# Optimization experiments

Hardware: AMD Instinct MI355X
Metric: run time of the kernel (lower is better)

## Reference

```python
import jax, jax.numpy as jnp
import numpy as np

B, S, D = 8, 2048, 256


def setup_inputs() -> dict:
    key = jax.random.key(0)
    ks = jax.random.split(key, 8)
    sc = 0.05
    return {
        "q": jax.random.normal(ks[0], (B, S, D), jnp.float32),
        "k": jax.random.normal(ks[1], (B, S, D), jnp.float32),
        "v": jax.random.normal(ks[2], (B, S, D), jnp.float32),
        "Wi0": jax.random.normal(ks[3], (D, D), jnp.float32) * sc,
        "Wi1": jax.random.normal(ks[4], (D, D), jnp.float32) * sc,
        "Wo0": jax.random.normal(ks[5], (D, D), jnp.float32) * sc,
        "Wo1": jax.random.normal(ks[6], (D, D), jnp.float32) * sc,
        "bo0": jnp.zeros((D,), jnp.float32),
        "bo1": jnp.zeros((D,), jnp.float32),
    }


def reference(q, k, v, Wi0, Wi1, Wo0, Wo1, bo0, bo1):
    d = q.shape[-1]
    scale = 1.0 / np.sqrt(d).astype(np.float32)
    # (B, S, S) shared score matrix
    scores = jnp.einsum("bqd,bkd->bqk", q, k) * scale
    s = scores.shape[-1]
    i = jnp.arange(s)[:, None]
    j = jnp.arange(s)[None, :]
    NEG = jnp.float32(-1e9)
    # fw: mask strictly-lower triangle (attend to j >= i); bw: mask strictly-upper (j <= i)
    fw_w = jax.nn.softmax(jnp.where(j < i, NEG, scores), axis=-1)
    bw_w = jax.nn.softmax(jnp.where(j > i, NEG, scores), axis=-1)
    fw_v = jnp.einsum("bqk,bkd->bqd", fw_w, v)
    bw_v = jnp.einsum("bqk,bkd->bqd", bw_w, v)
    # fusion gates: sigmoid(in_gate(v) + out_gate(att_v))  (torch Linear: x @ W.T + b)
    fw_gate = jax.nn.sigmoid(v @ Wi0.T + fw_v @ Wo0.T + bo0)
    bw_gate = jax.nn.sigmoid(v @ Wi1.T + bw_v @ Wo1.T + bo1)
    fw_out = fw_gate * fw_v + (1.0 - fw_gate) * v
    bw_out = bw_gate * bw_v + (1.0 - bw_gate) * v
    return jnp.concatenate((fw_out, bw_out), axis=-1)
```

## Files before the change

kernel.cpp:

```cpp
#include <hip/hip_runtime.h>
#include <stdint.h>


typedef unsigned short u16;
typedef unsigned int u32;
typedef __attribute__((ext_vector_type(8))) short short8;
typedef __attribute__((ext_vector_type(4))) float f32x4;

#define B_ 8
#define S_ 2048
#define D_ 256
#define QB 64
#define NP 32

#define LOG2E 1.44269504088896340736f
#define QSCALE (LOG2E/16.0f)
#define KSWZ_OFF 0
#define VT_OFF   (8u<<20)
#define WBF_OFF  (16u<<20)

__device__ __forceinline__ u16 f2bf(float f) {
    union { float f; u32 u; } x; x.f = f;
    u32 u = x.u + 0x7fffu + ((x.u >> 16) & 1u);
    return (u16)(u >> 16);
}
__device__ __forceinline__ float fget(float4 v, int i) {
    return i == 0 ? v.x : i == 1 ? v.y : i == 2 ? v.z : v.w;
}
__device__ __forceinline__ short8 pack8(float4 a, float4 b) {
    short8 r;
    r[0] = (short)f2bf(a.x); r[1] = (short)f2bf(a.y);
    r[2] = (short)f2bf(a.z); r[3] = (short)f2bf(a.w);
    r[4] = (short)f2bf(b.x); r[5] = (short)f2bf(b.y);
    r[6] = (short)f2bf(b.z); r[7] = (short)f2bf(b.w);
    return r;
}
__device__ __forceinline__ f32x4 mfma16(short8 a, short8 b, f32x4 c) {
    return __builtin_amdgcn_mfma_f32_16x16x32_bf16(a, b, c, 0, 0, 0);
}
__device__ __forceinline__ void gload_lds(const void* g, void* lds) {
    __builtin_amdgcn_global_load_lds(
        (const __attribute__((address_space(1))) void*)g,
        (__attribute__((address_space(3))) void*)lds, 16, 0, 0);
}

__global__ __launch_bounds__(256, 1)
void prep_kernel(const float* __restrict__ k, const float* __restrict__ v,
                 const float* __restrict__ w0, const float* __restrict__ w1,
                 const float* __restrict__ w2, const float* __restrict__ w3,
                 char* __restrict__ ws)
{
    const int tid = (int)threadIdx.x;
    const int bid = (int)blockIdx.x;

    if (bid < 512) {
        __shared__ float vs[32][257];
        const int b = bid >> 6, jt = bid & 63;
        const float* vb = v + ((size_t)b * S_ + (size_t)jt * 32) * D_;
        const int j = tid >> 3, d0 = (tid & 7) * 32;
        #pragma unroll
        for (int i = 0; i < 8; ++i) {
            float4 x = *(const float4*)(vb + (size_t)j * D_ + d0 + i * 4);
            vs[j][d0 + i * 4 + 0] = x.x; vs[j][d0 + i * 4 + 1] = x.y;
            vs[j][d0 + i * 4 + 2] = x.z; vs[j][d0 + i * 4 + 3] = x.w;
        }
        __syncthreads();
        u16* outp = (u16*)(ws + VT_OFF) + (size_t)(b * 64 + jt) * 8192 + (size_t)tid * 32;
        short8 o[4];
        #pragma unroll
        for (int jj = 0; jj < 32; ++jj) o[jj >> 3][jj & 7] = (short)f2bf(vs[jj][tid]);
        #pragma unroll
        for (int i = 0; i < 4; ++i) *(short8*)(outp + i * 8) = o[i];
    } else if (bid < 1024) {
        const int t = bid - 512, b = t >> 6, jt = t & 63;
        const float* kb = k + ((size_t)b * S_ + (size_t)jt * 32) * D_;
        char* ob = ws + KSWZ_OFF + (size_t)(b * 64 + jt) * 16384;
        #pragma unroll
        for (int it = 0; it < 4; ++it) {
            int gi = tid + it * 256;
            int r = gi >> 5, cg = gi & 31;
            float4 x0 = *(const float4*)(kb + (size_t)r * D_ + cg * 8);
            float4 x1 = *(const float4*)(kb + (size_t)r * D_ + cg * 8 + 4);
            *(short8*)(ob + r * 512 + ((cg * 16) ^ ((r & 7) << 4))) = pack8(x0, x1);
        }
    } else {
        const int t = bid - 1024, m = t >> 4, db = t & 15;
        const float* wsrc = (m == 0 ? w0 : m == 1 ? w1 : m == 2 ? w2 : w3)
                            + (size_t)(db * 16) * D_;
        char* ob = ws + WBF_OFF + (size_t)(db * 4 + m) * 8192;
        #pragma unroll
        for (int it = 0; it < 2; ++it) {
            int gi = tid + it * 256;
            int r = gi >> 5, cg = gi & 31;
            float4 x0 = *(const float4*)(wsrc + (size_t)r * D_ + cg * 8);
            float4 x1 = *(const float4*)(wsrc + (size_t)r * D_ + cg * 8 + 4);
            *(short8*)(ob + r * 512 + ((cg * 16) ^ ((r & 7) << 4))) = pack8(x0, x1);
        }
    }
}

#define PV_TAIL(accD, accS)                                                    \
    {                                                                          \
        short8 pa = *(const short8*)&pw[c * 40 + g * 8];                       \
        __builtin_amdgcn_s_setprio(1);                                         \
        accS = mfma16(pa, onesb, accS);                                        \
        _Pragma("unroll")                                                      \
        for (int db = 0; db < 16; ++db) {                                      \
            short8 vb = *(const short8*)(vcur + (db * 16 + c) * 64 + g * 16);  \
            accD[db] = mfma16(pa, vb, accD[db]);                               \
        }                                                                      \
        __builtin_amdgcn_s_setprio(0);                                         \
    }

#define DO_FULL(accD, accS)                                                    \
    {                                                                          \
        _Pragma("unroll")                                                      \
        for (int r = 0; r < 4; ++r) {                                          \
            pw[(g * 4 + r) * 40 + c]      = f2bf(exp2f(sc0[r]));               \
            pw[(g * 4 + r) * 40 + 16 + c] = f2bf(exp2f(sc1[r]));               \
        }                                                                      \
        PV_TAIL(accD, accS)                                                    \
    }

#define DO_MASK(CMPOP, accD, accS)                                             \
    {                                                                          \
        _Pragma("unroll")                                                      \
        for (int r = 0; r < 4; ++r) {                                          \
            int qq = r0 + g * 4 + r;                                           \
            float e0 = ((j0 + c) CMPOP qq) ? exp2f(sc0[r]) : 0.0f;             \
            float e1 = ((j0 + 16 + c) CMPOP qq) ? exp2f(sc1[r]) : 0.0f;        \
            pw[(g * 4 + r) * 40 + c]      = f2bf(e0);                          \
            pw[(g * 4 + r) * 40 + 16 + c] = f2bf(e1);                          \
        }                                                                      \
        PV_TAIL(accD, accS)                                                    \
    }

__global__ __launch_bounds__(512, 2)
void attn_kernel(const float* __restrict__ q, const char* __restrict__ kswz,
                 const char* __restrict__ vt, const char* __restrict__ wbf,
                 const float* __restrict__ v,
                 const float* __restrict__ bo0, const float* __restrict__ bo1,
                 float* __restrict__ out)
{
    __shared__ char smem[141824];
    u16* kbL = (u16*)smem;
    char* vtA = smem + 65536;
    u16* pl = (u16*)(smem + 131072);

    const int tid = (int)threadIdx.x;
    const int wv = tid >> 6, lane = tid & 63;
    const int h = wv >> 2, wl = wv & 3;
    const int g = lane >> 4, c = lane & 15;
    const int bid = (int)blockIdx.x;
    const int b = bid & 7, qi = bid >> 3;
    const int q0 = qi * QB;
    const int r0 = q0 + wl * 16;
    const int dt = r0 >> 5;
    u16* pw = pl + wv * 640;

    const char* kbase = kswz + (size_t)b * (64 * 16384);
    const char* vbase = vt + (size_t)b * (64 * 16384);

    short8 qf[8];
    {
        const float* qp = q + ((size_t)b * S_ + (size_t)(r0 + c)) * D_;
        #pragma unroll
        for (int ks = 0; ks < 8; ++ks) {
            float4 a = *(const float4*)(qp + ks * 32 + g * 8);
            float4 d = *(const float4*)(qp + ks * 32 + g * 8 + 4);
            a.x *= QSCALE; a.y *= QSCALE; a.z *= QSCALE; a.w *= QSCALE;
            d.x *= QSCALE; d.y *= QSCALE; d.z *= QSCALE; d.w *= QSCALE;
            qf[ks] = pack8(a, d);
        }
    }

    short8 onesb;
    #pragma unroll
    for (int i = 0; i < 8; ++i) onesb[i] = (c == 0) ? (short)0x3F80 : (short)0;

    const f32x4 zero4 = {0.f, 0.f, 0.f, 0.f};
    f32x4 accF[16], accB[16], accSF = zero4, accSB = zero4;
    #pragma unroll
    for (int i = 0; i < 16; ++i) { accF[i] = zero4; accB[i] = zero4; }

    #define STAGE(t, buf)                                                      \
        {                                                                      \
            const char* kg = kbase + (size_t)(t) * 32768;                      \
            const char* vg = vbase + (size_t)(t) * 32768;                      \
            _Pragma("unroll")                                                  \
            for (int i = 0; i < 4; ++i) {                                      \
                int off = i * 8192 + wv * 1024;                                \
                gload_lds(kg + off + lane * 16, (char*)kbL + (buf) * 32768 + off); \
                gload_lds(vg + off + lane * 16, vtA + (buf) * 32768 + off);    \
            }                                                                  \
        }

    STAGE(0, 0);
    __syncthreads();

    const int swz = (c & 7) << 4;

    #pragma unroll 1
    for (int t = 0; t < NP; ++t) {
        const int cur = t & 1;
        if (t + 1 < NP) STAGE(t + 1, cur ^ 1);

        const int jw = 2 * t + h;
        const int j0 = jw * 32;
        const char* kcur = (const char*)kbL + cur * 32768 + h * 16384;
        const char* vcur = vtA + cur * 32768 + h * 16384;

        f32x4 sc0 = zero4, sc1 = zero4;
        __builtin_amdgcn_s_setprio(1);
        #pragma unroll
        for (int ks = 0; ks < 8; ++ks) {
            int inner = (ks * 64 + g * 16) ^ swz;
            short8 kb0 = *(const short8*)(kcur + c * 512 + inner);
            short8 kb1 = *(const short8*)(kcur + (16 + c) * 512 + inner);
            sc0 = mfma16(qf[ks], kb0, sc0);
            sc1 = mfma16(qf[ks], kb1, sc1);
        }
        __builtin_amdgcn_s_setprio(0);

        if (jw < dt) {
            DO_FULL(accB, accSB)
        } else if (jw > dt) {
            DO_FULL(accF, accSF)
        } else {
            DO_MASK(<=, accB, accSB)
            DO_MASK(>=, accF, accSF)
        }
        __syncthreads();
    }

    float* sumsA = (float*)(smem + 131072);
    float* sumsB = (float*)(smem + 131072 + 256);

    if (h == 1) {
        float* dst = (float*)smem + wl * 4096;
        #pragma unroll
        for (int db = 0; db < 16; ++db)
            #pragma unroll
            for (int r = 0; r < 4; ++r)
                dst[(g * 4 + r) * 256 + db * 16 + c] = accF[db][r];
        if (c == 0) {
            #pragma unroll
            for (int r = 0; r < 4; ++r) sumsA[wl * 16 + g * 4 + r] = accSF[r];
        }
    } else {
        float* dst = (float*)vtA + wl * 4096;
        #pragma unroll
        for (int db = 0; db < 16; ++db)
            #pragma unroll
            for (int r = 0; r < 4; ++r)
                dst[(g * 4 + r) * 256 + db * 16 + c] = accB[db][r];
        if (c == 0) {
            #pragma unroll
            for (int r = 0; r < 4; ++r) sumsB[wl * 16 + g * 4 + r] = accSB[r];
        }
    }
    __syncthreads();

    f32x4 merged[16];
    if (h == 0) {
        const float* src = (const float*)smem + wl * 4096;
        float rs[4];
        #pragma unroll
        for (int r = 0; r < 4; ++r) {
            float so = __shfl(accSF[r], lane & 48);
            rs[r] = 1.0f / (so + sumsA[wl * 16 + g * 4 + r]);
        }
        #pragma unroll
        for (int db = 0; db < 16; ++db)
            #pragma unroll
            for (int r = 0; r < 4; ++r)
                merged[db][r] = (accF[db][r] + src[(g * 4 + r) * 256 + db * 16 + c]) * rs[r];
    } else {
        const float* src = (const float*)vtA + wl * 4096;
        float rs[4];
        #pragma unroll
        for (int r = 0; r < 4; ++r) {
            float so = __shfl(accSB[r], lane & 48);
            rs[r] = 1.0f / (so + sumsB[wl * 16 + g * 4 + r]);
        }
        #pragma unroll
        for (int db = 0; db < 16; ++db)
            #pragma unroll
            for (int r = 0; r < 4; ++r)
                merged[db][r] = (accB[db][r] + src[(g * 4 + r) * 256 + db * 16 + c]) * rs[r];
    }
    __syncthreads();

    {
        char* imgb = smem + h * 32768;
        #pragma unroll
        for (int db = 0; db < 16; ++db)
            #pragma unroll
            for (int r = 0; r < 4; ++r) {
                int lr = wl * 16 + g * 4 + r;
                int cb = (db * 16 + c) * 2;
                *(u16*)(imgb + lr * 512 + (cb ^ ((lr & 7) << 4))) = f2bf(merged[db][r]);
            }
    }
    #define WSTAGE(db, buf)                                                    \
        {                                                                      \
            const char* gsrc = wbf + (size_t)(db) * 32768;                     \
            _Pragma("unroll")                                                  \
            for (int i = 0; i < 4; ++i) {                                      \
                int off = i * 8192 + wv * 1024;                                \
                gload_lds(gsrc + off + lane * 16, vtA + (buf) * 32768 + off);  \
            }                                                                  \
        }
    WSTAGE(0, 0);
    __syncthreads();

    short8 af[8], vf[8];
    {
        const char* imgb = smem + h * 32768;
        int lr = wl * 16 + c;
        #pragma unroll
        for (int ks = 0; ks < 8; ++ks) {
            int inner = (ks * 64 + g * 16) ^ swz;
            af[ks] = *(const short8*)(imgb + lr * 512 + inner);
        }
        const float* vp = v + ((size_t)b * S_ + (size_t)(r0 + c)) * D_;
        #pragma unroll
        for (int ks = 0; ks < 8; ++ks) {
            float4 a = *(const float4*)(vp + ks * 32 + g * 8);
            float4 d = *(const float4*)(vp + ks * 32 + g * 8 + 4);
            vf[ks] = pack8(a, d);
        }
    }

    const float* bias = (h == 0) ? bo0 : bo1;
    const float* vrow = v + ((size_t)b * S_ + (size_t)r0) * D_;
    float* ob = out + ((size_t)b * S_ + (size_t)r0) * 512 + h * 256;
    #pragma unroll
    for (int db = 0; db < 16; ++db) {
        const int cu2 = db & 1;
        if (db + 1 < 16) WSTAGE(db + 1, cu2 ^ 1);

        float bb = bias[db * 16 + c];
        f32x4 a = {bb, bb, bb, bb};
        const char* wc = vtA + cu2 * 32768 + h * 16384;
        __builtin_amdgcn_s_setprio(1);
        #pragma unroll
        for (int ks = 0; ks < 8; ++ks) {
            int inner = (ks * 64 + g * 16) ^ swz;
            short8 wi = *(const short8*)(wc + c * 512 + inner);
            short8 wo = *(const short8*)(wc + 8192 + c * 512 + inner);
            a = mfma16(vf[ks], wi, a);
            a = mfma16(af[ks], wo, a);
        }
        __builtin_amdgcn_s_setprio(0);

        #pragma unroll
        for (int r = 0; r < 4; ++r) {
            int row = g * 4 + r;
            float vv = vrow[(size_t)row * D_ + db * 16 + c];
            float gate = 1.0f / (1.0f + exp2f(-a[r] * LOG2E));
            float m = merged[db][r];
            ob[(size_t)row * 512 + db * 16 + c] = gate * m + (1.0f - gate) * vv;
        }
        __syncthreads();
    }
}

extern "C" void kernel_launch(void* const* d_in, const int* in_sizes, int n_in,
                              void* d_out, int out_size, void* d_ws, size_t ws_size,
                              hipStream_t stream)
{
    const float* q   = (const float*)d_in[0];
    const float* k   = (const float*)d_in[1];
    const float* v   = (const float*)d_in[2];
    const float* Wi0 = (const float*)d_in[3];
    const float* Wi1 = (const float*)d_in[4];
    const float* Wo0 = (const float*)d_in[5];
    const float* Wo1 = (const float*)d_in[6];
    const float* bo0 = (const float*)d_in[7];
    const float* bo1 = (const float*)d_in[8];
    float* out = (float*)d_out;
    char* ws = (char*)d_ws;
    (void)in_sizes; (void)n_in; (void)ws_size; (void)out_size;

    prep_kernel<<<dim3(1088), dim3(256), 0, stream>>>(k, v, Wi0, Wo0, Wi1, Wo1, ws);
    attn_kernel<<<dim3(256), dim3(512), 0, stream>>>(q, ws + KSWZ_OFF, ws + VT_OFF,
                                                     ws + WBF_OFF, v, bo0, bo1, out);
}
```

Measured before the change: 99.24 us.

## Software-pipeline PV one tile behind QK and pad V layout against bank conflicts

Restructures the main attention loop so the P·V MFMAs for tile t-1 run in the same iteration as the QK^T scores for tile t. P is double-buffered per wave, and V loads are staged separately from K loads. The transposed-V workspace and the LDS P buffers gain padding (72-byte and 36-element row strides) to reduce LDS bank conflicts, read as two 8-byte halves. The diagonal tile now writes both masked variants in one pass. The cost is more LDS (about 154 KB), which may limit occupancy, plus an extra epilogue PV step.

Measured after the change: 111.7 us. +12.6%, slower.

```diff
diff --git a/kernel.cpp b/kernel.cpp
--- a/kernel.cpp
+++ b/kernel.cpp
@@ -5,6 +5,7 @@
 typedef unsigned short u16;
 typedef unsigned int u32;
 typedef __attribute__((ext_vector_type(8))) short short8;
+typedef __attribute__((ext_vector_type(4))) short short4v;
 typedef __attribute__((ext_vector_type(4))) float f32x4;
 
 #define B_ 8
@@ -15,17 +16,20 @@
 
 #define LOG2E 1.44269504088896340736f
 #define QSCALE (LOG2E/16.0f)
+
 #define KSWZ_OFF 0
 #define VT_OFF   (8u<<20)
-#define WBF_OFF  (16u<<20)
+#define VT_BATCH 1179648u
+#define WBF_OFF  (VT_OFF + 8u*VT_BATCH)
+
+#define LDS_K  0
+#define LDS_V  65536
+#define LDS_P  139264
 
 __device__ __forceinline__ u16 f2bf(float f) {
     union { float f; u32 u; } x; x.f = f;
     u32 u = x.u + 0x7fffu + ((x.u >> 16) & 1u);
     return (u16)(u >> 16);
-}
-__device__ __forceinline__ float fget(float4 v, int i) {
-    return i == 0 ? v.x : i == 1 ? v.y : i == 2 ? v.z : v.w;
 }
 __device__ __forceinline__ short8 pack8(float4 a, float4 b) {
     short8 r;
@@ -65,12 +69,13 @@
             vs[j][d0 + i * 4 + 2] = x.z; vs[j][d0 + i * 4 + 3] = x.w;
         }
         __syncthreads();
-        u16* outp = (u16*)(ws + VT_OFF) + (size_t)(b * 64 + jt) * 8192 + (size_t)tid * 32;
+        char* ob = ws + VT_OFF + (size_t)b * VT_BATCH + (size_t)(jt >> 1) * 36864
+                   + (size_t)(jt & 1) * 18432 + (size_t)tid * 72;
         short8 o[4];
         #pragma unroll
         for (int jj = 0; jj < 32; ++jj) o[jj >> 3][jj & 7] = (short)f2bf(vs[jj][tid]);
         #pragma unroll
-        for (int i = 0; i < 4; ++i) *(short8*)(outp + i * 8) = o[i];
+        for (int i = 0; i < 4; ++i) *(short8*)(ob + i * 16) = o[i];
     } else if (bid < 1024) {
         const int t = bid - 512, b = t >> 6, jt = t & 63;
         const float* kb = k + ((size_t)b * S_ + (size_t)jt * 32) * D_;
@@ -99,40 +104,23 @@
     }
 }
 
-#define PV_TAIL(accD, accS)                                                    \
+#define PV_DO(pslot, vptr, accD, accS)                                         \
     {                                                                          \
-        short8 pa = *(const short8*)&pw[c * 40 + g * 8];                       \
+        const u16* pp_ = (pslot);                                              \
+        short4v plo_ = *(const short4v*)(pp_ + c * 36 + g * 8);                \
+        short4v phi_ = *(const short4v*)(pp_ + c * 36 + g * 8 + 4);            \
+        short8 pa_ = __builtin_shufflevector(plo_, phi_, 0,1,2,3,4,5,6,7);     \
         __builtin_amdgcn_s_setprio(1);                                         \
-        accS = mfma16(pa, onesb, accS);                                        \
+        accS = mfma16(pa_, onesb, accS);                                       \
         _Pragma("unroll")                                                      \
         for (int db = 0; db < 16; ++db) {                                      \
-            short8 vb = *(const short8*)(vcur + (db * 16 + c) * 64 + g * 16);  \
-            accD[db] = mfma16(pa, vb, accD[db]);                               \
+            const char* vp_ = (vptr) + (db * 16 + c) * 72 + g * 16;            \
+            short4v vlo_ = *(const short4v*)(vp_);                             \
+            short4v vhi_ = *(const short4v*)(vp_ + 8);                         \
+            short8 vb_ = __builtin_shufflevector(vlo_, vhi_, 0,1,2,3,4,5,6,7); \
+            accD[db] = mfma16(pa_, vb_, accD[db]);                             \
         }                                                                      \
         __builtin_amdgcn_s_setprio(0);                                         \
-    }
-
-#define DO_FULL(accD, accS)                                                    \
-    {                                                                          \
-        _Pragma("unroll")                                                      \
-        for (int r = 0; r < 4; ++r) {                                          \
-            pw[(g * 4 + r) * 40 + c]      = f2bf(exp2f(sc0[r]));               \
-            pw[(g * 4 + r) * 40 + 16 + c] = f2bf(exp2f(sc1[r]));               \
-        }                                                                      \
-        PV_TAIL(accD, accS)                                                    \
-    }
-
-#define DO_MASK(CMPOP, accD, accS)                                             \
-    {                                                                          \
-        _Pragma("unroll")                                                      \
-        for (int r = 0; r < 4; ++r) {                                          \
-            int qq = r0 + g * 4 + r;                                           \
-            float e0 = ((j0 + c) CMPOP qq) ? exp2f(sc0[r]) : 0.0f;             \
-            float e1 = ((j0 + 16 + c) CMPOP qq) ? exp2f(sc1[r]) : 0.0f;        \
-            pw[(g * 4 + r) * 40 + c]      = f2bf(e0);                          \
-            pw[(g * 4 + r) * 40 + 16 + c] = f2bf(e1);                          \
-        }                                                                      \
-        PV_TAIL(accD, accS)                                                    \
     }
 
 __global__ __launch_bounds__(512, 2)
@@ -142,10 +130,7 @@
                  const float* __restrict__ bo0, const float* __restrict__ bo1,
                  float* __restrict__ out)
 {
-    __shared__ char smem[141824];
-    u16* kbL = (u16*)smem;
-    char* vtA = smem + 65536;
-    u16* pl = (u16*)(smem + 131072);
+    __shared__ char smem[157696];
 
     const int tid = (int)threadIdx.x;
     const int wv = tid >> 6, lane = tid & 63;
@@ -156,10 +141,11 @@
     const int q0 = qi * QB;
     const int r0 = q0 + wl * 16;
     const int dt = r0 >> 5;
-    u16* pw = pl + wv * 640;
-
-    const char* kbase = kswz + (size_t)b * (64 * 16384);
-    const char* vbase = vt + (size_t)b * (64 * 16384);
+
+    u16* pwave = (u16*)(smem + LDS_P) + wv * 1152;
+
+    const char* kbaseg = kswz + (size_t)b * (64 * 16384);
+    const char* vbaseg = vt + (size_t)b * VT_BATCH;
 
     short8 qf[8];
     {
@@ -183,19 +169,29 @@
     #pragma unroll
     for (int i = 0; i < 16; ++i) { accF[i] = zero4; accB[i] = zero4; }
 
-    #define STAGE(t, buf)                                                      \
+    #define STAGE_K(t, buf)                                                    \
         {                                                                      \
-            const char* kg = kbase + (size_t)(t) * 32768;                      \
-            const char* vg = vbase + (size_t)(t) * 32768;                      \
+            const char* kg_ = kbaseg + (size_t)(t) * 32768;                    \
             _Pragma("unroll")                                                  \
             for (int i = 0; i < 4; ++i) {                                      \
                 int off = i * 8192 + wv * 1024;                                \
-                gload_lds(kg + off + lane * 16, (char*)kbL + (buf) * 32768 + off); \
-                gload_lds(vg + off + lane * 16, vtA + (buf) * 32768 + off);    \
+                gload_lds(kg_ + off + lane * 16, smem + LDS_K + (buf) * 32768 + off); \
             }                                                                  \
         }
-
-    STAGE(0, 0);
+    #define STAGE_V(t, buf)                                                    \
+        {                                                                      \
+            const char* vg_ = vbaseg + (size_t)(t) * 36864;                    \
+            _Pragma("unroll")                                                  \
+            for (int i = 0; i < 4; ++i) {                                      \
+                int off = i * 8192 + wv * 1024;                                \
+                gload_lds(vg_ + off + lane * 16, smem + LDS_V + (buf) * 36864 + off); \
+            }                                                                  \
+            if (wv < 4)                                                        \
+                gload_lds(vg_ + 32768 + wv * 1024 + lane * 16,                 \
+                          smem + LDS_V + (buf) * 36864 + 32768 + wv * 1024);   \
+        }
+
+    STAGE_K(0, 0);
     __syncthreads();
 
     const int swz = (c & 7) << 4;
@@ -203,13 +199,20 @@
     #pragma unroll 1
     for (int t = 0; t < NP; ++t) {
         const int cur = t & 1;
-        if (t + 1 < NP) STAGE(t + 1, cur ^ 1);
-
-        const int jw = 2 * t + h;
-        const int j0 = jw * 32;
-        const char* kcur = (const char*)kbL + cur * 32768 + h * 16384;
-        const char* vcur = vtA + cur * 32768 + h * 16384;
-
+        if (t + 1 < NP) STAGE_K(t + 1, cur ^ 1);
+        STAGE_V(t, cur);
+
+        if (t > 0) {
+            const int tp = t - 1, sp = tp & 1, jwp = 2 * tp + h;
+            const u16* pP = pwave + sp * 576;
+            const char* vP = smem + LDS_V + sp * 36864 + h * 18432;
+            if (jwp < dt) { PV_DO(pP, vP, accB, accSB); }
+            else if (jwp > dt) { PV_DO(pP, vP, accF, accSF); }
+            else { PV_DO(pP, vP, accB, accSB);
+                   PV_DO(pwave + (sp ^ 1) * 576, vP, accF, accSF); }
+        }
+
+        const char* kcur = smem + LDS_K + cur * 32768 + h * 16384;
         f32x4 sc0 = zero4, sc1 = zero4;
         __builtin_amdgcn_s_setprio(1);
         #pragma unroll
@@ -222,19 +225,43 @@
         }
         __builtin_amdgcn_s_setprio(0);
 
-        if (jw < dt) {
-            DO_FULL(accB, accSB)
-        } else if (jw > dt) {
-            DO_FULL(accF, accSF)
+        const int jw = 2 * t + h, j0 = jw * 32;
+        u16* pc = pwave + cur * 576;
+        if (jw == dt) {
+            u16* pf = pwave + (cur ^ 1) * 576;
+            #pragma unroll
+            for (int r = 0; r < 4; ++r) {
+                int row = g * 4 + r, qq = r0 + row;
+                float e0 = exp2f(sc0[r]), e1 = exp2f(sc1[r]);
+                pc[row * 36 + c]      = f2bf((j0 + c) <= qq ? e0 : 0.0f);
+                pc[row * 36 + 16 + c] = f2bf((j0 + 16 + c) <= qq ? e1 : 0.0f);
+                pf[row * 36 + c]      = f2bf((j0 + c) >= qq ? e0 : 0.0f);
+                pf[row * 36 + 16 + c] = f2bf((j0 + 16 + c) >= qq ? e1 : 0.0f);
+            }
         } else {
-            DO_MASK(<=, accB, accSB)
-            DO_MASK(>=, accF, accSF)
+            #pragma unroll
+            for (int r = 0; r < 4; ++r) {
+                int row = g * 4 + r;
+                pc[row * 36 + c]      = f2bf(exp2f(sc0[r]));
+                pc[row * 36 + 16 + c] = f2bf(exp2f(sc1[r]));
+            }
         }
         __syncthreads();
     }
 
-    float* sumsA = (float*)(smem + 131072);
-    float* sumsB = (float*)(smem + 131072 + 256);
+    {
+        const int tp = NP - 1, sp = tp & 1, jwp = 2 * tp + h;
+        const u16* pP = pwave + sp * 576;
+        const char* vP = smem + LDS_V + sp * 36864 + h * 18432;
+        if (jwp < dt) { PV_DO(pP, vP, accB, accSB); }
+        else if (jwp > dt) { PV_DO(pP, vP, accF, accSF); }
+        else { PV_DO(pP, vP, accB, accSB);
+               PV_DO(pwave + (sp ^ 1) * 576, vP, accF, accSF); }
+    }
+    __syncthreads();
+
+    float* sumsA = (float*)(smem + LDS_P);
+    float* sumsB = (float*)(smem + LDS_P + 256);
 
     if (h == 1) {
         float* dst = (float*)smem + wl * 4096;
@@ -248,7 +275,7 @@
             for (int r = 0; r < 4; ++r) sumsA[wl * 16 + g * 4 + r] = accSF[r];
         }
     } else {
-        float* dst = (float*)vtA + wl * 4096;
+        float* dst = (float*)(smem + LDS_V) + wl * 4096;
         #pragma unroll
         for (int db = 0; db < 16; ++db)
             #pragma unroll
@@ -276,7 +303,7 @@
             for (int r = 0; r < 4; ++r)
                 merged[db][r] = (accF[db][r] + src[(g * 4 + r) * 256 + db * 16 + c]) * rs[r];
     } else {
-        const float* src = (const float*)vtA + wl * 4096;
+        const float* src = (const float*)(smem + LDS_V) + wl * 4096;
         float rs[4];
         #pragma unroll
         for (int r = 0; r < 4; ++r) {
@@ -308,7 +335,8 @@
             _Pragma("unroll")                                                  \
             for (int i = 0; i < 4; ++i) {                                      \
                 int off = i * 8192 + wv * 1024;                                \
-                gload_lds(gsrc + off + lane * 16, vtA + (buf) * 32768 + off);  \
+                gload_lds(gsrc + off + lane * 16,                              \
+                          smem + LDS_V + (buf) * 32768 + off);                 \
             }                                                                  \
         }
     WSTAGE(0, 0);
@@ -342,7 +370,7 @@
 
         float bb = bias[db * 16 + c];
         f32x4 a = {bb, bb, bb, bb};
-        const char* wc = vtA + cu2 * 32768 + h * 16384;
+        const char* wc = smem + LDS_V + cu2 * 32768 + h * 16384;
         __builtin_amdgcn_s_setprio(1);
         #pragma unroll
         for (int ks = 0; ks < 8; ++ks) {
```

## Switch attention to 32x32 MFMA with register-resident P and direct V loads

Applied to the files above, without the earlier changes.

Rewrites the attention kernel around 32x32x16 bf16 MFMAs. Each wave now covers a 32-query by 32-key tile and half of the D columns. Probabilities are packed to bf16 in registers with cvt_pk and permlane32_swap instead of being round-tripped through LDS. Row sums are accumulated in scalars rather than through an extra ones-MFMA. V fragments are read straight from a prepacked global image rather than staged into LDS, and the prep kernel now emits fragment-ordered K and V images. This aims to cut LDS traffic and MFMA issue count, but it adds a cross-wave reduction of partial accumulators and global-latency exposure on the V loads. The merged attention output is stored as bf16 in LDS for the gate stage, which loses some precision relative to the fp32 values used before.

Measured after the change: 179.7 us. 81.1% more time.

```diff
diff --git a/kernel.cpp b/kernel.cpp
--- a/kernel.cpp
+++ b/kernel.cpp
@@ -6,26 +6,24 @@
 typedef unsigned int u32;
 typedef __attribute__((ext_vector_type(8))) short short8;
 typedef __attribute__((ext_vector_type(4))) float f32x4;
+typedef __attribute__((ext_vector_type(16))) float f32x16;
 
 #define B_ 8
 #define S_ 2048
 #define D_ 256
-#define QB 64
 #define NP 32
 
 #define LOG2E 1.44269504088896340736f
 #define QSCALE (LOG2E/16.0f)
-#define KSWZ_OFF 0
-#define VT_OFF   (8u<<20)
+
+#define KIMG_OFF 0u
+#define VIMG_OFF (8u<<20)
 #define WBF_OFF  (16u<<20)
 
 __device__ __forceinline__ u16 f2bf(float f) {
     union { float f; u32 u; } x; x.f = f;
     u32 u = x.u + 0x7fffu + ((x.u >> 16) & 1u);
     return (u16)(u >> 16);
-}
-__device__ __forceinline__ float fget(float4 v, int i) {
-    return i == 0 ? v.x : i == 1 ? v.y : i == 2 ? v.z : v.w;
 }
 __device__ __forceinline__ short8 pack8(float4 a, float4 b) {
     short8 r;
@@ -37,6 +35,17 @@
 }
 __device__ __forceinline__ f32x4 mfma16(short8 a, short8 b, f32x4 c) {
     return __builtin_amdgcn_mfma_f32_16x16x32_bf16(a, b, c, 0, 0, 0);
+}
+__device__ __forceinline__ f32x16 mfma32(short8 a, short8 b, f32x16 c) {
+    return __builtin_amdgcn_mfma_f32_32x32x16_bf16(a, b, c, 0, 0, 0);
+}
+__device__ __forceinline__ u32 pk2(float a, float b) {
+    u32 w;
+    asm("v_cvt_pk_bf16_f32 %0, %1, %2" : "=v"(w) : "v"(a), "v"(b));
+    return w;
+}
+__device__ __forceinline__ void plswap(u32& a, u32& b) {
+    asm volatile("v_permlane32_swap_b32 %0, %1" : "+v"(a), "+v"(b));
 }
 __device__ __forceinline__ void gload_lds(const void* g, void* lds) {
     __builtin_amdgcn_global_load_lds(
@@ -53,35 +62,38 @@
     const int tid = (int)threadIdx.x;
     const int bid = (int)blockIdx.x;
 
-    if (bid < 512) {
-        __shared__ float vs[32][257];
-        const int b = bid >> 6, jt = bid & 63;
-        const float* vb = v + ((size_t)b * S_ + (size_t)jt * 32) * D_;
-        const int j = tid >> 3, d0 = (tid & 7) * 32;
+    if (bid < 1024) {
+        __shared__ float st[32][264];
+        const bool isV = (bid < 512);
+        const int t = isV ? bid : bid - 512;
+        const int b = t >> 6, jb = t & 63;
+        const float* src = (isV ? v : k) + ((size_t)b * S_ + (size_t)jb * 32) * D_;
+        const int jr = tid >> 3, d0 = (tid & 7) * 32;
         #pragma unroll
         for (int i = 0; i < 8; ++i) {
-            float4 x = *(const float4*)(vb + (size_t)j * D_ + d0 + i * 4);
-            vs[j][d0 + i * 4 + 0] = x.x; vs[j][d0 + i * 4 + 1] = x.y;
-            vs[j][d0 + i * 4 + 2] = x.z; vs[j][d0 + i * 4 + 3] = x.w;
+            float4 x = *(const float4*)(src + (size_t)jr * D_ + d0 + i * 4);
+            *(float4*)&st[jr][d0 + i * 4] = x;
         }
         __syncthreads();
-        u16* outp = (u16*)(ws + VT_OFF) + (size_t)(b * 64 + jt) * 8192 + (size_t)tid * 32;
-        short8 o[4];
-        #pragma unroll
-        for (int jj = 0; jj < 32; ++jj) o[jj >> 3][jj & 7] = (short)f2bf(vs[jj][tid]);
-        #pragma unroll
-        for (int i = 0; i < 4; ++i) *(short8*)(outp + i * 8) = o[i];
-    } else if (bid < 1024) {
-        const int t = bid - 512, b = t >> 6, jt = t & 63;
-        const float* kb = k + ((size_t)b * S_ + (size_t)jt * 32) * D_;
-        char* ob = ws + KSWZ_OFF + (size_t)(b * 64 + jt) * 16384;
+        char* ob = ws + (isV ? VIMG_OFF : KIMG_OFF)
+                 + ((size_t)b * 64 + jb) * 16384;
         #pragma unroll
         for (int it = 0; it < 4; ++it) {
-            int gi = tid + it * 256;
-            int r = gi >> 5, cg = gi & 31;
-            float4 x0 = *(const float4*)(kb + (size_t)r * D_ + cg * 8);
-            float4 x1 = *(const float4*)(kb + (size_t)r * D_ + cg * 8 + 4);
-            *(short8*)(ob + r * 512 + ((cg * 16) ^ ((r & 7) << 4))) = pack8(x0, x1);
+            int e = it * 256 + tid;
+            int fi = e >> 6, l = e & 63;
+            short8 o;
+            if (isV) {
+                int db = fi >> 1, ks2 = fi & 1;
+                int row = ks2 * 16 + (l >> 5) * 8, col = db * 32 + (l & 31);
+                #pragma unroll
+                for (int i = 0; i < 8; ++i) o[i] = (short)f2bf(st[row + i][col]);
+            } else {
+                int ks = fi;
+                int row = l & 31, col = ks * 16 + (l >> 5) * 8;
+                #pragma unroll
+                for (int i = 0; i < 8; ++i) o[i] = (short)f2bf(st[row][col + i]);
+            }
+            *(short8*)(ob + e * 16) = o;
         }
     } else {
         const int t = bid - 1024, m = t >> 4, db = t & 15;
@@ -99,207 +111,204 @@
     }
 }
 
-#define PV_TAIL(accD, accS)                                                    \
-    {                                                                          \
-        short8 pa = *(const short8*)&pw[c * 40 + g * 8];                       \
-        __builtin_amdgcn_s_setprio(1);                                         \
-        accS = mfma16(pa, onesb, accS);                                        \
-        _Pragma("unroll")                                                      \
-        for (int db = 0; db < 16; ++db) {                                      \
-            short8 vb = *(const short8*)(vcur + (db * 16 + c) * 64 + g * 16);  \
-            accD[db] = mfma16(pa, vb, accD[db]);                               \
-        }                                                                      \
-        __builtin_amdgcn_s_setprio(0);                                         \
-    }
-
-#define DO_FULL(accD, accS)                                                    \
-    {                                                                          \
-        _Pragma("unroll")                                                      \
-        for (int r = 0; r < 4; ++r) {                                          \
-            pw[(g * 4 + r) * 40 + c]      = f2bf(exp2f(sc0[r]));               \
-            pw[(g * 4 + r) * 40 + 16 + c] = f2bf(exp2f(sc1[r]));               \
-        }                                                                      \
-        PV_TAIL(accD, accS)                                                    \
-    }
-
-#define DO_MASK(CMPOP, accD, accS)                                             \
-    {                                                                          \
-        _Pragma("unroll")                                                      \
-        for (int r = 0; r < 4; ++r) {                                          \
-            int qq = r0 + g * 4 + r;                                           \
-            float e0 = ((j0 + c) CMPOP qq) ? exp2f(sc0[r]) : 0.0f;             \
-            float e1 = ((j0 + 16 + c) CMPOP qq) ? exp2f(sc1[r]) : 0.0f;        \
-            pw[(g * 4 + r) * 40 + c]      = f2bf(e0);                          \
-            pw[(g * 4 + r) * 40 + 16 + c] = f2bf(e1);                          \
-        }                                                                      \
-        PV_TAIL(accD, accS)                                                    \
-    }
+union PaU { u32 w[4]; short8 s; };
 
 __global__ __launch_bounds__(512, 2)
-void attn_kernel(const float* __restrict__ q, const char* __restrict__ kswz,
-                 const char* __restrict__ vt, const char* __restrict__ wbf,
+void attn_kernel(const float* __restrict__ q, const char* __restrict__ kimg,
+                 const char* __restrict__ vimg, const char* __restrict__ wbf,
                  const float* __restrict__ v,
                  const float* __restrict__ bo0, const float* __restrict__ bo1,
                  float* __restrict__ out)
 {
-    __shared__ char smem[141824];
-    u16* kbL = (u16*)smem;
-    char* vtA = smem + 65536;
-    u16* pl = (u16*)(smem + 131072);
+    __shared__ char smem[133632];
 
     const int tid = (int)threadIdx.x;
     const int wv = tid >> 6, lane = tid & 63;
-    const int h = wv >> 2, wl = wv & 3;
-    const int g = lane >> 4, c = lane & 15;
+    const int qh = wv & 1, jh = (wv >> 1) & 1, dh = wv >> 2;
+    const int h = lane >> 5, ln = lane & 31;
+    const int g = (lane & 63) >> 4, c = lane & 15;
     const int bid = (int)blockIdx.x;
     const int b = bid & 7, qi = bid >> 3;
-    const int q0 = qi * QB;
-    const int r0 = q0 + wl * 16;
-    const int dt = r0 >> 5;
-    u16* pw = pl + wv * 640;
-
-    const char* kbase = kswz + (size_t)b * (64 * 16384);
-    const char* vbase = vt + (size_t)b * (64 * 16384);
-
-    short8 qf[8];
+    const int q0 = qi * 64;
+    const int qb = qi * 2 + qh;
+    const int qg = q0 + qh * 32 + ln;
+
+    const char* kbaseg = kimg + ((size_t)b << 20);
+    const char* vbaseg = vimg + ((size_t)b << 20);
+
+    short8 qf[16];
     {
-        const float* qp = q + ((size_t)b * S_ + (size_t)(r0 + c)) * D_;
-        #pragma unroll
-        for (int ks = 0; ks < 8; ++ks) {
-            float4 a = *(const float4*)(qp + ks * 32 + g * 8);
-            float4 d = *(const float4*)(qp + ks * 32 + g * 8 + 4);
+        const float* qp = q + ((size_t)b * S_ + (size_t)(q0 + qh * 32 + ln)) * D_ + h * 8;
+        #pragma unroll
+        for (int ks = 0; ks < 16; ++ks) {
+            float4 a = *(const float4*)(qp + ks * 16);
+            float4 d = *(const float4*)(qp + ks * 16 + 4);
             a.x *= QSCALE; a.y *= QSCALE; a.z *= QSCALE; a.w *= QSCALE;
             d.x *= QSCALE; d.y *= QSCALE; d.z *= QSCALE; d.w *= QSCALE;
             qf[ks] = pack8(a, d);
         }
     }
 
-    short8 onesb;
-    #pragma unroll
-    for (int i = 0; i < 8; ++i) onesb[i] = (c == 0) ? (short)0x3F80 : (short)0;
-
-    const f32x4 zero4 = {0.f, 0.f, 0.f, 0.f};
-    f32x4 accF[16], accB[16], accSF = zero4, accSB = zero4;
-    #pragma unroll
-    for (int i = 0; i < 16; ++i) { accF[i] = zero4; accB[i] = zero4; }
-
-    #define STAGE(t, buf)                                                      \
+    f32x16 accF[4] = {}, accB[4] = {};
+    float sF = 0.0f, sB = 0.0f;
+
+    #define STAGE_K(t, buf)                                                    \
         {                                                                      \
-            const char* kg = kbase + (size_t)(t) * 32768;                      \
-            const char* vg = vbase + (size_t)(t) * 32768;                      \
+            const char* kg_ = kbaseg + (size_t)(t) * 32768;                    \
             _Pragma("unroll")                                                  \
             for (int i = 0; i < 4; ++i) {                                      \
                 int off = i * 8192 + wv * 1024;                                \
-                gload_lds(kg + off + lane * 16, (char*)kbL + (buf) * 32768 + off); \
-                gload_lds(vg + off + lane * 16, vtA + (buf) * 32768 + off);    \
+                gload_lds(kg_ + off + lane * 16, smem + (buf) * 32768 + off);  \
             }                                                                  \
         }
 
-    STAGE(0, 0);
+    STAGE_K(0, 0);
     __syncthreads();
 
-    const int swz = (c & 7) << 4;
+    #define PVALL(pa0_, pa1_, acc_)                                            \
+        {                                                                      \
+            __builtin_amdgcn_s_setprio(1);                                     \
+            acc_[0] = mfma32(pa0_, vb0a, acc_[0]);                             \
+            acc_[0] = mfma32(pa1_, vb0b, acc_[0]);                             \
+            acc_[1] = mfma32(pa0_, vb1a, acc_[1]);                             \
+            acc_[1] = mfma32(pa1_, vb1b, acc_[1]);                             \
+            acc_[2] = mfma32(pa0_, vb2a, acc_[2]);                             \
+            acc_[2] = mfma32(pa1_, vb2b, acc_[2]);                             \
+            acc_[3] = mfma32(pa0_, vb3a, acc_[3]);                             \
+            acc_[3] = mfma32(pa1_, vb3b, acc_[3]);                             \
+            __builtin_amdgcn_s_setprio(0);                                     \
+        }
+
+    #define REPACK(e_, pa0_, pa1_)                                             \
+        {                                                                      \
+            u32 w0 = pk2(e_[0], e_[1]),  w1 = pk2(e_[2], e_[3]);               \
+            u32 w2 = pk2(e_[4], e_[5]),  w3 = pk2(e_[6], e_[7]);               \
+            u32 w4 = pk2(e_[8], e_[9]),  w5 = pk2(e_[10], e_[11]);             \
+            u32 w6 = pk2(e_[12], e_[13]), w7 = pk2(e_[14], e_[15]);            \
+            plswap(w0, w2); plswap(w1, w3); plswap(w4, w6); plswap(w5, w7);    \
+            PaU u0_; u0_.w[0] = w0; u0_.w[1] = w1; u0_.w[2] = w2; u0_.w[3] = w3; \
+            PaU u1_; u1_.w[0] = w4; u1_.w[1] = w5; u1_.w[2] = w6; u1_.w[3] = w7; \
+            pa0_ = u0_.s; pa1_ = u1_.s;                                        \
+        }
+
+    #define SUM16(e_) ((((e_[0]+e_[1])+(e_[2]+e_[3]))+((e_[4]+e_[5])+(e_[6]+e_[7]))) + \
+                       (((e_[8]+e_[9])+(e_[10]+e_[11]))+((e_[12]+e_[13])+(e_[14]+e_[15]))))
 
     #pragma unroll 1
     for (int t = 0; t < NP; ++t) {
         const int cur = t & 1;
-        if (t + 1 < NP) STAGE(t + 1, cur ^ 1);
-
-        const int jw = 2 * t + h;
-        const int j0 = jw * 32;
-        const char* kcur = (const char*)kbL + cur * 32768 + h * 16384;
-        const char* vcur = vtA + cur * 32768 + h * 16384;
-
-        f32x4 sc0 = zero4, sc1 = zero4;
+        if (t + 1 < NP) STAGE_K(t + 1, cur ^ 1);
+
+        const int jbg = 2 * t + jh;
+        const char* vg = vbaseg + (size_t)jbg * 16384 + dh * 8192 + lane * 16;
+
+        short8 vb0a = *(const short8*)(vg);
+        short8 vb0b = *(const short8*)(vg + 1024);
+        short8 vb1a = *(const short8*)(vg + 2048);
+        short8 vb1b = *(const short8*)(vg + 3072);
+
+        const char* kc_ = smem + cur * 32768 + jh * 16384 + lane * 16;
+        f32x16 sc = {};
         __builtin_amdgcn_s_setprio(1);
         #pragma unroll
-        for (int ks = 0; ks < 8; ++ks) {
-            int inner = (ks * 64 + g * 16) ^ swz;
-            short8 kb0 = *(const short8*)(kcur + c * 512 + inner);
-            short8 kb1 = *(const short8*)(kcur + (16 + c) * 512 + inner);
-            sc0 = mfma16(qf[ks], kb0, sc0);
-            sc1 = mfma16(qf[ks], kb1, sc1);
+        for (int ks = 0; ks < 16; ++ks) {
+            short8 kb = *(const short8*)(kc_ + ks * 1024);
+            sc = mfma32(kb, qf[ks], sc);
         }
         __builtin_amdgcn_s_setprio(0);
 
-        if (jw < dt) {
-            DO_FULL(accB, accSB)
-        } else if (jw > dt) {
-            DO_FULL(accF, accSF)
+        short8 vb2a = *(const short8*)(vg + 4096);
+        short8 vb2b = *(const short8*)(vg + 5120);
+        short8 vb3a = *(const short8*)(vg + 6144);
+        short8 vb3b = *(const short8*)(vg + 7168);
+
+        #pragma unroll
+        for (int i = 0; i < 16; ++i) sc[i] = exp2f(sc[i]);
+
+        if (jbg != qb) {
+            float e[16];
+            #pragma unroll
+            for (int i = 0; i < 16; ++i) e[i] = sc[i];
+            short8 pa0, pa1;
+            REPACK(e, pa0, pa1);
+            float ts = SUM16(e);
+            if (jbg < qb) { sB += ts; PVALL(pa0, pa1, accB); }
+            else          { sF += ts; PVALL(pa0, pa1, accF); }
         } else {
-            DO_MASK(<=, accB, accSB)
-            DO_MASK(>=, accF, accSF)
+            const int jb32 = jbg * 32;
+            {
+                float e[16];
+                #pragma unroll
+                for (int r = 0; r < 16; ++r) {
+                    int jg = jb32 + (r & 3) + 8 * (r >> 2) + 4 * h;
+                    e[r] = (jg <= qg) ? sc[r] : 0.0f;
+                }
+                short8 pa0, pa1;
+                REPACK(e, pa0, pa1);
+                sB += SUM16(e);
+                PVALL(pa0, pa1, accB);
+            }
+            {
+                float e[16];
+                #pragma unroll
+                for (int r = 0; r < 16; ++r) {
+                    int jg = jb32 + (r & 3) + 8 * (r >> 2) + 4 * h;
+                    e[r] = (jg >= qg) ? sc[r] : 0.0f;
+                }
+                short8 pa0, pa1;
+                REPACK(e, pa0, pa1);
+                sF += SUM16(e);
+                PVALL(pa0, pa1, accF);
+            }
         }
         __syncthreads();
     }
 
-    float* sumsA = (float*)(smem + 131072);
-    float* sumsB = (float*)(smem + 131072 + 256);
-
-    if (h == 1) {
-        float* dst = (float*)smem + wl * 4096;
-        #pragma unroll
-        for (int db = 0; db < 16; ++db)
+    {
+        float* dst = (float*)(smem + (jh ? 0 : 65536)) + (qh * 2 + dh) * 4096;
+        #pragma unroll
+        for (int db = 0; db < 4; ++db)
             #pragma unroll
-            for (int r = 0; r < 4; ++r)
-                dst[(g * 4 + r) * 256 + db * 16 + c] = accF[db][r];
-        if (c == 0) {
+            for (int r = 0; r < 16; ++r)
+                dst[(db * 16 + r) * 64 + lane] = jh ? accF[db][r] : accB[db][r];
+        if (dh == 0) {
+            ((float*)(smem + 131072))[(qh * 2 + jh) * 64 + lane] = sF;
+            ((float*)(smem + 132096))[(qh * 2 + jh) * 64 + lane] = sB;
+        }
+    }
+    __syncthreads();
+
+    {
+        const float* src = (const float*)(smem + (jh ? 65536 : 0)) + (qh * 2 + dh) * 4096;
+        #pragma unroll
+        for (int db = 0; db < 4; ++db)
             #pragma unroll
-            for (int r = 0; r < 4; ++r) sumsA[wl * 16 + g * 4 + r] = accSF[r];
-        }
-    } else {
-        float* dst = (float*)vtA + wl * 4096;
-        #pragma unroll
-        for (int db = 0; db < 16; ++db)
+            for (int r = 0; r < 16; ++r) {
+                float p = src[(db * 16 + r) * 64 + lane];
+                if (jh) accB[db][r] += p; else accF[db][r] += p;
+            }
+        if (jh == 0 && dh == 0) {
+            const float* pf = (const float*)(smem + (h ? 132096 : 131072));
+            int qq = ln;
+            float s = pf[(qh * 2 + 0) * 64 + qq] + pf[(qh * 2 + 0) * 64 + 32 + qq]
+                    + pf[(qh * 2 + 1) * 64 + qq] + pf[(qh * 2 + 1) * 64 + 32 + qq];
+            ((float*)(smem + 133120))[h * 64 + qh * 32 + qq] = 1.0f / s;
+        }
+    }
+    __syncthreads();
+
+    {
+        const float* rsp = (const float*)(smem + 133120) + jh * 64;
+        char* imgb = smem + jh * 32768;
+        #pragma unroll
+        for (int db = 0; db < 4; ++db)
             #pragma unroll
-            for (int r = 0; r < 4; ++r)
-                dst[(g * 4 + r) * 256 + db * 16 + c] = accB[db][r];
-        if (c == 0) {
-            #pragma unroll
-            for (int r = 0; r < 4; ++r) sumsB[wl * 16 + g * 4 + r] = accSB[r];
-        }
-    }
-    __syncthreads();
-
-    f32x4 merged[16];
-    if (h == 0) {
-        const float* src = (const float*)smem + wl * 4096;
-        float rs[4];
-        #pragma unroll
-        for (int r = 0; r < 4; ++r) {
-            float so = __shfl(accSF[r], lane & 48);
-            rs[r] = 1.0f / (so + sumsA[wl * 16 + g * 4 + r]);
-        }
-        #pragma unroll
-        for (int db = 0; db < 16; ++db)
-            #pragma unroll
-            for (int r = 0; r < 4; ++r)
-                merged[db][r] = (accF[db][r] + src[(g * 4 + r) * 256 + db * 16 + c]) * rs[r];
-    } else {
-        const float* src = (const float*)vtA + wl * 4096;
-        float rs[4];
-        #pragma unroll
-        for (int r = 0; r < 4; ++r) {
-            float so = __shfl(accSB[r], lane & 48);
-            rs[r] = 1.0f / (so + sumsB[wl * 16 + g * 4 + r]);
-        }
-        #pragma unroll
-        for (int db = 0; db < 16; ++db)
-            #pragma unroll
-            for (int r = 0; r < 4; ++r)
-                merged[db][r] = (accB[db][r] + src[(g * 4 + r) * 256 + db * 16 + c]) * rs[r];
-    }
-    __syncthreads();
-
-    {
-        char* imgb = smem + h * 32768;
-        #pragma unroll
-        for (int db = 0; db < 16; ++db)
-            #pragma unroll
-            for (int r = 0; r < 4; ++r) {
-                int lr = wl * 16 + g * 4 + r;
-                int cb = (db * 16 + c) * 2;
-                *(u16*)(imgb + lr * 512 + (cb ^ ((lr & 7) << 4))) = f2bf(merged[db][r]);
+            for (int r = 0; r < 16; ++r) {
+                int qib = (r & 3) + 8 * (r >> 2) + 4 * h;
+                float m = (jh ? accB[db][r] : accF[db][r]) * rsp[qh * 32 + qib];
+                int row = qh * 32 + qib;
+                int dcol = dh * 128 + db * 32 + ln;
+                *(u16*)(imgb + row * 512 + ((2 * dcol) ^ ((row & 7) << 4))) = f2bf(m);
             }
     }
     #define WSTAGE(db, buf)                                                    \
@@ -308,22 +317,25 @@
             _Pragma("unroll")                                                  \
             for (int i = 0; i < 4; ++i) {                                      \
                 int off = i * 8192 + wv * 1024;                                \
-                gload_lds(gsrc + off + lane * 16, vtA + (buf) * 32768 + off);  \
+                gload_lds(gsrc + off + lane * 16,                              \
+                          smem + 65536 + (buf) * 32768 + off);                 \
             }                                                                  \
         }
     WSTAGE(0, 0);
     __syncthreads();
 
+    const int wl2 = qh * 2 + dh;
+    const int swz = (c & 7) << 4;
     short8 af[8], vf[8];
     {
-        const char* imgb = smem + h * 32768;
-        int lr = wl * 16 + c;
+        const char* imgb = smem + jh * 32768;
+        int lr = wl2 * 16 + c;
         #pragma unroll
         for (int ks = 0; ks < 8; ++ks) {
-            int inner = (ks * 64 + g * 16) ^ swz;
+            int inner = (ks * 64 + g * 16) ^ ((lr & 7) << 4);
             af[ks] = *(const short8*)(imgb + lr * 512 + inner);
         }
-        const float* vp = v + ((size_t)b * S_ + (size_t)(r0 + c)) * D_;
+        const float* vp = v + ((size_t)b * S_ + (size_t)(q0 + wl2 * 16 + c)) * D_;
         #pragma unroll
         for (int ks = 0; ks < 8; ++ks) {
             float4 a = *(const float4*)(vp + ks * 32 + g * 8);
@@ -332,9 +344,10 @@
         }
     }
 
-    const float* bias = (h == 0) ? bo0 : bo1;
-    const float* vrow = v + ((size_t)b * S_ + (size_t)r0) * D_;
-    float* ob = out + ((size_t)b * S_ + (size_t)r0) * 512 + h * 256;
+    const float* bias = jh ? bo1 : bo0;
+    const float* vrow = v + ((size_t)b * S_ + (size_t)(q0 + wl2 * 16)) * D_;
+    const char* imgb2 = smem + jh * 32768;
+    float* ob = out + ((size_t)b * S_ + (size_t)(q0 + wl2 * 16)) * 512 + jh * 256;
     #pragma unroll
     for (int db = 0; db < 16; ++db) {
         const int cu2 = db & 1;
@@ -342,7 +355,7 @@
 
         float bb = bias[db * 16 + c];
         f32x4 a = {bb, bb, bb, bb};
-        const char* wc = vtA + cu2 * 32768 + h * 16384;
+        const char* wc = smem + 65536 + cu2 * 32768 + jh * 16384;
         __builtin_amdgcn_s_setprio(1);
         #pragma unroll
         for (int ks = 0; ks < 8; ++ks) {
@@ -356,11 +369,13 @@
 
         #pragma unroll
         for (int r = 0; r < 4; ++r) {
-            int row = g * 4 + r;
-            float vv = vrow[(size_t)row * D_ + db * 16 + c];
+            int row = wl2 * 16 + g * 4 + r;
+            int cc = db * 16 + c;
+            float vv = vrow[(size_t)(g * 4 + r) * D_ + cc];
+            u32 mu = *(const u16*)(imgb2 + row * 512 + ((2 * cc) ^ ((row & 7) << 4)));
+            union { u32 u; float f; } cv; cv.u = mu << 16;
             float gate = 1.0f / (1.0f + exp2f(-a[r] * LOG2E));
-            float m = merged[db][r];
-            ob[(size_t)row * 512 + db * 16 + c] = gate * m + (1.0f - gate) * vv;
+            ob[(size_t)(g * 4 + r) * 512 + cc] = gate * cv.f + (1.0f - gate) * vv;
         }
         __syncthreads();
     }
@@ -384,6 +399,6 @@
     (void)in_sizes; (void)n_in; (void)ws_size; (void)out_size;
 
     prep_kernel<<<dim3(1088), dim3(256), 0, stream>>>(k, v, Wi0, Wo0, Wi1, Wo1, ws);
-    attn_kernel<<<dim3(256), dim3(512), 0, stream>>>(q, ws + KSWZ_OFF, ws + VT_OFF,
+    attn_kernel<<<dim3(256), dim3(512), 0, stream>>>(q, ws + KIMG_OFF, ws + VIMG_OFF,
                                                      ws + WBF_OFF, v, bo0, bo1, out);
 }
```
